# Kernel tuning notes

Hardware: AMD Instinct MI355X
Metric: run time of the kernel (lower is better)

## Reference

```python
import jax, jax.numpy as jnp
import numpy as np

IN_DIM, HID, OUT_DIM, BATCH, T = 512, 1024, 512, 4096, 32

def setup_inputs() -> dict:
    key = jax.random.key(0)
    ks = jax.random.split(key, 7)
    s_in = 1.0 / np.sqrt(IN_DIM)
    s_h = 1.0 / np.sqrt(HID)
    return {
        "x": jax.random.normal(ks[0], (IN_DIM, BATCH), dtype=jnp.float32),
        "W_in": jax.random.normal(ks[1], (HID, IN_DIM), dtype=jnp.float32) * s_in,
        "b_in": jax.random.normal(ks[2], (HID, 1), dtype=jnp.float32) * 0.01,
        "W_rec": jax.random.normal(ks[3], (HID, HID), dtype=jnp.float32) * s_h,
        "b_rec": jax.random.normal(ks[4], (HID, 1), dtype=jnp.float32) * 0.01,
        "W_out": jax.random.normal(ks[5], (OUT_DIM, HID), dtype=jnp.float32) * s_h,
        "b_out": jax.random.normal(ks[6], (OUT_DIM, 1), dtype=jnp.float32) * 0.01,
    }

def reference(x, W_in, b_in, W_rec, b_rec, W_out, b_out):
    # initial projection: [H, B]
    y0 = jax.nn.relu(W_in @ x + b_in)

    def step(h, _):
        h_next = jax.nn.relu(W_rec @ h + b_rec)
        return h_next, h_next

    h_last, hs = jax.lax.scan(step, y0, None, length=T)  # hs: [T, H, B]
    out = jax.nn.relu(W_out @ h_last + b_out)  # [O, B]
    intermediate = jnp.concatenate([y0[None], hs], axis=0)  # [T+1, H, B]
    return out, intermediate
```

## Files before the change

kernel.cpp:

```cpp
#include <hip/hip_runtime.h>
#include <hip/hip_bf16.h>

#define IN_DIM  512
#define HID     1024
#define OUT_DIM 512
#define BATCH   4096
#define T_STEPS 32

typedef __attribute__((ext_vector_type(8))) short bf16x8;
typedef __attribute__((ext_vector_type(4))) float f32x4;

__device__ inline void gload16(const void* g, void* l) {
  __builtin_amdgcn_global_load_lds(
      (const __attribute__((address_space(1))) void*)g,
      (__attribute__((address_space(3))) void*)l, 16, 0, 0);
}

__device__ inline void bload(bf16x8 &d, const __hip_bfloat16* p) {
  asm volatile("global_load_dwordx4 %0, %1, off"
               : "=&v"(d) : "v"(p) : "memory");
}

__global__ __launch_bounds__(256, 2) void gemm_bt_bias_relu(
    const __hip_bfloat16* __restrict__ A,
    const __hip_bfloat16* __restrict__ Wt,
    const float* __restrict__ bias,
    float* __restrict__ Cf,
    __hip_bfloat16* __restrict__ Cb,
    int K, int Nld, int nx)
{
  const int nwg = gridDim.x;
  const int q   = nwg >> 3;
  const int bid = blockIdx.x;
  const int swz = (bid & 7) * q + (bid >> 3);
  const int bxi = swz % nx;
  const int byi = swz / nx;
  const int brow = byi * 128;
  const int bcol = bxi * 64;

  const int tid  = threadIdx.x;
  const int lane = tid & 63;
  const int wid  = tid >> 6;
  const int wr   = wid >> 1, wc = wid & 1;
  const int l15  = lane & 15, l4 = lane >> 4;
  const int srow = lane >> 3;
  const int schunk = (lane & 7) ^ (srow & 7);

  __shared__ __hip_bfloat16 Alds[2][128 * 64];

  f32x4 acc[4][2] = {};
  const int nt = K >> 6;

  auto stageA = [&](int ti, int buf) {
    const int kt = ti << 6;
#pragma unroll
    for (int it = 0; it < 4; ++it) {
      const int rowbase = it * 32 + wid * 8;
      gload16(A + (size_t)(brow + rowbase + srow) * K + kt + schunk * 8,
              &Alds[buf][rowbase * 64]);
    }
  };

  const int Ks = K >> 5;
  const __hip_bfloat16* wt[2];
  wt[0] = Wt + (size_t)((bcol >> 4) + wc * 2 + 0) * Ks * 512 + lane * 8;
  wt[1] = Wt + (size_t)((bcol >> 4) + wc * 2 + 1) * Ks * 512 + lane * 8;

  bf16x8 bx[2][2], by[2][2];

#pragma unroll
  for (int n = 0; n < 2; ++n) {
    bload(bx[n][0], wt[n] + 0 * 512);
    bload(bx[n][1], wt[n] + 1 * 512);
  }
  __builtin_amdgcn_sched_barrier(0);
  stageA(0, 0);
  __builtin_amdgcn_sched_barrier(0);
#pragma unroll
  for (int n = 0; n < 2; ++n) {
    bload(by[n][0], wt[n] + 2 * 512);
    bload(by[n][1], wt[n] + 3 * 512);
  }
  __builtin_amdgcn_sched_barrier(0);
  stageA(1, 1);

  const int rxor = l15 & 7;

  auto iterf = [&](int ti, bf16x8 (&cb)[2][2]) {
    const int buf = ti & 1;
    if (ti < nt - 1) {
      asm volatile("s_waitcnt vmcnt(8)" ::: "memory");
    } else {
      asm volatile("s_waitcnt vmcnt(0)" ::: "memory");
    }
    __builtin_amdgcn_s_barrier();
    __builtin_amdgcn_sched_barrier(0);

    __builtin_amdgcn_s_setprio(1);
#pragma unroll
    for (int ks = 0; ks < 2; ++ks) {
      bf16x8 af[4];
      const int cp = ((ks * 4 + l4) ^ rxor) * 8;
#pragma unroll
      for (int m = 0; m < 4; ++m)
        af[m] = *(const bf16x8*)&Alds[buf][(wr * 64 + m * 16 + l15) * 64 + cp];
#pragma unroll
      for (int m = 0; m < 4; ++m)
#pragma unroll
        for (int n = 0; n < 2; ++n)
          acc[m][n] = __builtin_amdgcn_mfma_f32_16x16x32_bf16(af[m], cb[n][ks], acc[m][n], 0, 0, 0);
    }
    __builtin_amdgcn_s_setprio(0);
    __builtin_amdgcn_sched_barrier(0);

    if (ti + 2 < nt) {
      const int s0 = (ti + 2) * 2;
#pragma unroll
      for (int n = 0; n < 2; ++n) {
        bload(cb[n][0], wt[n] + (s0 + 0) * 512);
        bload(cb[n][1], wt[n] + (s0 + 1) * 512);
      }
    }

    asm volatile("s_waitcnt lgkmcnt(0)" ::: "memory");
    __builtin_amdgcn_sched_barrier(0);
    __builtin_amdgcn_s_barrier();
    __builtin_amdgcn_sched_barrier(0);
    if (ti + 2 < nt) stageA(ti + 2, buf);
  };

  for (int ti = 0; ti < nt; ti += 2) {
    iterf(ti,     bx);
    iterf(ti + 1, by);
  }

#pragma unroll
  for (int n = 0; n < 2; ++n) {
    const int i = bcol + wc * 32 + n * 16 + l15;
    const float bv = bias[i];
#pragma unroll
    for (int m = 0; m < 4; ++m) {
      const int b0 = brow + wr * 64 + m * 16 + l4 * 4;
      f32x4 v = acc[m][n];
      f32x4 o;
      o[0] = fmaxf(v[0] + bv, 0.0f);
      o[1] = fmaxf(v[1] + bv, 0.0f);
      o[2] = fmaxf(v[2] + bv, 0.0f);
      o[3] = fmaxf(v[3] + bv, 0.0f);
      __builtin_nontemporal_store(o, (f32x4*)(Cf + (size_t)i * BATCH + b0));
      if (Cb) {
        Cb[(size_t)(b0 + 0) * Nld + i] = __float2bfloat16(o[0]);
        Cb[(size_t)(b0 + 1) * Nld + i] = __float2bfloat16(o[1]);
        Cb[(size_t)(b0 + 2) * Nld + i] = __float2bfloat16(o[2]);
        Cb[(size_t)(b0 + 3) * Nld + i] = __float2bfloat16(o[3]);
      }
    }
  }
}

__global__ __launch_bounds__(256) void convert_weights_tiled(
    const float* __restrict__ w_in, const float* __restrict__ w_rec,
    const float* __restrict__ w_out,
    __hip_bfloat16* __restrict__ wi, __hip_bfloat16* __restrict__ wr,
    __hip_bfloat16* __restrict__ wo)
{
  const int c  = blockIdx.x * blockDim.x + threadIdx.x;
  const int c1 = HID * IN_DIM / 8;
  const int c2 = c1 + HID * HID / 8;
  const int c3 = c2 + OUT_DIM * HID / 8;
  const float* src; __hip_bfloat16* dst; int K, local;
  if (c < c1)      { src = w_in;  dst = wi; K = IN_DIM; local = c; }
  else if (c < c2) { src = w_rec; dst = wr; K = HID;    local = c - c1; }
  else if (c < c3) { src = w_out; dst = wo; K = HID;    local = c - c2; }
  else return;
  const int kc8 = K >> 3;
  const int i  = local / kc8;
  const int k0 = (local - i * kc8) << 3;
  const float4 a = *(const float4*)(src + (size_t)i * K + k0);
  const float4 b = *(const float4*)(src + (size_t)i * K + k0 + 4);
  union { __hip_bfloat16 h[8]; bf16x8 v; } p;
  p.h[0] = __float2bfloat16(a.x); p.h[1] = __float2bfloat16(a.y);
  p.h[2] = __float2bfloat16(a.z); p.h[3] = __float2bfloat16(a.w);
  p.h[4] = __float2bfloat16(b.x); p.h[5] = __float2bfloat16(b.y);
  p.h[6] = __float2bfloat16(b.z); p.h[7] = __float2bfloat16(b.w);
  const size_t off = ((size_t)(i >> 4) * (K >> 5) + (k0 >> 5)) * 512
                   + ((k0 >> 3) & 3) * 128 + (i & 15) * 8;
  *(bf16x8*)(dst + off) = p.v;
}

__global__ __launch_bounds__(256) void transpose_f32_bf16(
    const float* __restrict__ in, __hip_bfloat16* __restrict__ out, int R, int C)
{
  __shared__ float tile[32][33];
  const int c0 = blockIdx.x * 32, r0 = blockIdx.y * 32;
  const int tx = threadIdx.x & 31, ty = threadIdx.x >> 5;
#pragma unroll
  for (int dy = 0; dy < 32; dy += 8)
    tile[ty + dy][tx] = in[(size_t)(r0 + ty + dy) * C + c0 + tx];
  __syncthreads();
#pragma unroll
  for (int dy = 0; dy < 32; dy += 8)
    out[(size_t)(c0 + ty + dy) * R + r0 + tx] = __float2bfloat16(tile[tx][ty + dy]);
}

extern "C" void kernel_launch(void* const* d_in, const int* in_sizes, int n_in,
                              void* d_out, int out_size, void* d_ws, size_t ws_size,
                              hipStream_t stream)
{
  const float* x     = (const float*)d_in[0];
  const float* W_in  = (const float*)d_in[1];
  const float* b_in  = (const float*)d_in[2];
  const float* W_rec = (const float*)d_in[3];
  const float* b_rec = (const float*)d_in[4];
  const float* W_out = (const float*)d_in[5];
  const float* b_out = (const float*)d_in[6];

  float* out0 = (float*)d_out;
  float* itm  = out0 + (size_t)OUT_DIM * BATCH;

  __hip_bfloat16* xT = (__hip_bfloat16*)d_ws;
  __hip_bfloat16* Wi = xT + (size_t)BATCH * IN_DIM;
  __hip_bfloat16* Wr = Wi + (size_t)HID * IN_DIM;
  __hip_bfloat16* Wo = Wr + (size_t)HID * HID;
  __hip_bfloat16* h0 = Wo + (size_t)OUT_DIM * HID;
  __hip_bfloat16* h1 = h0 + (size_t)BATCH * HID;

  transpose_f32_bf16<<<dim3(BATCH / 32, IN_DIM / 32), 256, 0, stream>>>(x, xT, IN_DIM, BATCH);
  {
    const int nC = (HID * IN_DIM + HID * HID + OUT_DIM * HID) / 8;
    convert_weights_tiled<<<(nC + 255) / 256, 256, 0, stream>>>(
        W_in, W_rec, W_out, Wi, Wr, Wo);
  }

  gemm_bt_bias_relu<<<(HID / 64) * (BATCH / 128), 256, 0, stream>>>(
      xT, Wi, b_in, itm, h0, IN_DIM, HID, HID / 64);

  __hip_bfloat16* cur = h0;
  __hip_bfloat16* nxt = h1;
  for (int t = 0; t < T_STEPS; ++t) {
    float* dst = itm + (size_t)(t + 1) * HID * BATCH;
    gemm_bt_bias_relu<<<(HID / 64) * (BATCH / 128), 256, 0, stream>>>(
        cur, Wr, b_rec, dst, nxt, HID, HID, HID / 64);
    __hip_bfloat16* tmp = cur; cur = nxt; nxt = tmp;
  }

  gemm_bt_bias_relu<<<(OUT_DIM / 64) * (BATCH / 128), 256, 0, stream>>>(
      cur, Wo, b_out, out0, (__hip_bfloat16*)nullptr, HID, 0, OUT_DIM / 64);
}
```

Baseline: 503.6 us.

## Store activations in MFMA-fragment layout and load both operands directly to registers

The bf16 activation buffers (the transposed input and the hidden states) are now written in the same fragment-tiled layout already used for the weights. The GEMM can therefore load both A and B fragments straight from global memory into registers, which removes the LDS staging, the swizzle and the workgroup barriers. The warp tiling changes so that each wave owns 32 rows by 64 columns. The cost is more global loads per wave with no LDS sharing of A across waves, plus scattered 2-byte stores in the epilogue.

Measured after the change: 584.9 us. +16.2%, slower.

```diff
diff --git a/kernel.cpp b/kernel.cpp
--- a/kernel.cpp
+++ b/kernel.cpp
@@ -10,24 +10,18 @@
 typedef __attribute__((ext_vector_type(8))) short bf16x8;
 typedef __attribute__((ext_vector_type(4))) float f32x4;
 
-__device__ inline void gload16(const void* g, void* l) {
-  __builtin_amdgcn_global_load_lds(
-      (const __attribute__((address_space(1))) void*)g,
-      (__attribute__((address_space(3))) void*)l, 16, 0, 0);
-}
-
-__device__ inline void bload(bf16x8 &d, const __hip_bfloat16* p) {
+__device__ inline void fload(bf16x8 &d, const __hip_bfloat16* p) {
   asm volatile("global_load_dwordx4 %0, %1, off"
                : "=&v"(d) : "v"(p) : "memory");
 }
 
-__global__ __launch_bounds__(256, 2) void gemm_bt_bias_relu(
-    const __hip_bfloat16* __restrict__ A,
+__global__ __launch_bounds__(256, 2) void gemm_ft(
+    const __hip_bfloat16* __restrict__ At,
     const __hip_bfloat16* __restrict__ Wt,
     const float* __restrict__ bias,
     float* __restrict__ Cf,
     __hip_bfloat16* __restrict__ Cb,
-    int K, int Nld, int nx)
+    int K, int nx)
 {
   const int nwg = gridDim.x;
   const int q   = nwg >> 3;
@@ -41,106 +35,72 @@
   const int tid  = threadIdx.x;
   const int lane = tid & 63;
   const int wid  = tid >> 6;
-  const int wr   = wid >> 1, wc = wid & 1;
   const int l15  = lane & 15, l4 = lane >> 4;
-  const int srow = lane >> 3;
-  const int schunk = (lane & 7) ^ (srow & 7);
-
-  __shared__ __hip_bfloat16 Alds[2][128 * 64];
-
-  f32x4 acc[4][2] = {};
+
+  const int Ks = K >> 5;
   const int nt = K >> 6;
 
-  auto stageA = [&](int ti, int buf) {
-    const int kt = ti << 6;
-#pragma unroll
-    for (int it = 0; it < 4; ++it) {
-      const int rowbase = it * 32 + wid * 8;
-      gload16(A + (size_t)(brow + rowbase + srow) * K + kt + schunk * 8,
-              &Alds[buf][rowbase * 64]);
-    }
+  const __hip_bfloat16* wa0 = At + (size_t)((brow >> 4) + wid * 2 + 0) * Ks * 512 + lane * 8;
+  const __hip_bfloat16* wa1 = At + (size_t)((brow >> 4) + wid * 2 + 1) * Ks * 512 + lane * 8;
+  const __hip_bfloat16* wb0 = Wt + (size_t)((bcol >> 4) + 0) * Ks * 512 + lane * 8;
+  const __hip_bfloat16* wb1 = Wt + (size_t)((bcol >> 4) + 1) * Ks * 512 + lane * 8;
+  const __hip_bfloat16* wb2 = Wt + (size_t)((bcol >> 4) + 2) * Ks * 512 + lane * 8;
+  const __hip_bfloat16* wb3 = Wt + (size_t)((bcol >> 4) + 3) * Ks * 512 + lane * 8;
+
+  f32x4 acc[2][4] = {};
+
+  bf16x8 bX[4][2], aX[2][2];
+  bf16x8 bY[4][2], aY[2][2];
+
+  auto loadTile = [&](int ti, bf16x8 (&cb)[4][2], bf16x8 (&ca)[2][2]) {
+    const int s0 = ti * 2;
+    fload(cb[0][0], wb0 + (s0 + 0) * 512); fload(cb[0][1], wb0 + (s0 + 1) * 512);
+    fload(cb[1][0], wb1 + (s0 + 0) * 512); fload(cb[1][1], wb1 + (s0 + 1) * 512);
+    fload(cb[2][0], wb2 + (s0 + 0) * 512); fload(cb[2][1], wb2 + (s0 + 1) * 512);
+    fload(cb[3][0], wb3 + (s0 + 0) * 512); fload(cb[3][1], wb3 + (s0 + 1) * 512);
+    fload(ca[0][0], wa0 + (s0 + 0) * 512); fload(ca[0][1], wa0 + (s0 + 1) * 512);
+    fload(ca[1][0], wa1 + (s0 + 0) * 512); fload(ca[1][1], wa1 + (s0 + 1) * 512);
   };
 
-  const int Ks = K >> 5;
-  const __hip_bfloat16* wt[2];
-  wt[0] = Wt + (size_t)((bcol >> 4) + wc * 2 + 0) * Ks * 512 + lane * 8;
-  wt[1] = Wt + (size_t)((bcol >> 4) + wc * 2 + 1) * Ks * 512 + lane * 8;
-
-  bf16x8 bx[2][2], by[2][2];
-
-#pragma unroll
-  for (int n = 0; n < 2; ++n) {
-    bload(bx[n][0], wt[n] + 0 * 512);
-    bload(bx[n][1], wt[n] + 1 * 512);
-  }
-  __builtin_amdgcn_sched_barrier(0);
-  stageA(0, 0);
-  __builtin_amdgcn_sched_barrier(0);
-#pragma unroll
-  for (int n = 0; n < 2; ++n) {
-    bload(by[n][0], wt[n] + 2 * 512);
-    bload(by[n][1], wt[n] + 3 * 512);
-  }
-  __builtin_amdgcn_sched_barrier(0);
-  stageA(1, 1);
-
-  const int rxor = l15 & 7;
-
-  auto iterf = [&](int ti, bf16x8 (&cb)[2][2]) {
-    const int buf = ti & 1;
+  loadTile(0, bX, aX);
+  loadTile(1, bY, aY);
+
+  auto iterf = [&](int ti, bf16x8 (&cb)[4][2], bf16x8 (&ca)[2][2]) {
     if (ti < nt - 1) {
-      asm volatile("s_waitcnt vmcnt(8)" ::: "memory");
+      asm volatile("s_waitcnt vmcnt(12)" ::: "memory");
     } else {
       asm volatile("s_waitcnt vmcnt(0)" ::: "memory");
     }
-    __builtin_amdgcn_s_barrier();
     __builtin_amdgcn_sched_barrier(0);
 
     __builtin_amdgcn_s_setprio(1);
 #pragma unroll
-    for (int ks = 0; ks < 2; ++ks) {
-      bf16x8 af[4];
-      const int cp = ((ks * 4 + l4) ^ rxor) * 8;
-#pragma unroll
-      for (int m = 0; m < 4; ++m)
-        af[m] = *(const bf16x8*)&Alds[buf][(wr * 64 + m * 16 + l15) * 64 + cp];
-#pragma unroll
-      for (int m = 0; m < 4; ++m)
-#pragma unroll
-        for (int n = 0; n < 2; ++n)
-          acc[m][n] = __builtin_amdgcn_mfma_f32_16x16x32_bf16(af[m], cb[n][ks], acc[m][n], 0, 0, 0);
-    }
+    for (int ks = 0; ks < 2; ++ks)
+#pragma unroll
+      for (int m = 0; m < 2; ++m)
+#pragma unroll
+        for (int n = 0; n < 4; ++n)
+          acc[m][n] = __builtin_amdgcn_mfma_f32_16x16x32_bf16(
+              ca[m][ks], cb[n][ks], acc[m][n], 0, 0, 0);
     __builtin_amdgcn_s_setprio(0);
     __builtin_amdgcn_sched_barrier(0);
 
-    if (ti + 2 < nt) {
-      const int s0 = (ti + 2) * 2;
-#pragma unroll
-      for (int n = 0; n < 2; ++n) {
-        bload(cb[n][0], wt[n] + (s0 + 0) * 512);
-        bload(cb[n][1], wt[n] + (s0 + 1) * 512);
-      }
-    }
-
-    asm volatile("s_waitcnt lgkmcnt(0)" ::: "memory");
-    __builtin_amdgcn_sched_barrier(0);
-    __builtin_amdgcn_s_barrier();
-    __builtin_amdgcn_sched_barrier(0);
-    if (ti + 2 < nt) stageA(ti + 2, buf);
+    if (ti + 2 < nt) loadTile(ti + 2, cb, ca);
   };
 
   for (int ti = 0; ti < nt; ti += 2) {
-    iterf(ti,     bx);
-    iterf(ti + 1, by);
-  }
-
-#pragma unroll
-  for (int n = 0; n < 2; ++n) {
-    const int i = bcol + wc * 32 + n * 16 + l15;
+    iterf(ti,     bX, aX);
+    iterf(ti + 1, bY, aY);
+  }
+
+#pragma unroll
+  for (int n = 0; n < 4; ++n) {
+    const int i = bcol + n * 16 + l15;
     const float bv = bias[i];
-#pragma unroll
-    for (int m = 0; m < 4; ++m) {
-      const int b0 = brow + wr * 64 + m * 16 + l4 * 4;
+    const int ioff = (i >> 5) * 512 + ((i >> 3) & 3) * 128 + (i & 7);
+#pragma unroll
+    for (int m = 0; m < 2; ++m) {
+      const int b0 = brow + wid * 32 + m * 16 + l4 * 4;
       f32x4 v = acc[m][n];
       f32x4 o;
       o[0] = fmaxf(v[0] + bv, 0.0f);
@@ -149,10 +109,11 @@
       o[3] = fmaxf(v[3] + bv, 0.0f);
       __builtin_nontemporal_store(o, (f32x4*)(Cf + (size_t)i * BATCH + b0));
       if (Cb) {
-        Cb[(size_t)(b0 + 0) * Nld + i] = __float2bfloat16(o[0]);
-        Cb[(size_t)(b0 + 1) * Nld + i] = __float2bfloat16(o[1]);
-        Cb[(size_t)(b0 + 2) * Nld + i] = __float2bfloat16(o[2]);
-        Cb[(size_t)(b0 + 3) * Nld + i] = __float2bfloat16(o[3]);
+        const size_t cbase = (size_t)(b0 >> 4) * 16384 + ioff + l4 * 32;
+        Cb[cbase +  0] = __float2bfloat16(o[0]);
+        Cb[cbase +  8] = __float2bfloat16(o[1]);
+        Cb[cbase + 16] = __float2bfloat16(o[2]);
+        Cb[cbase + 24] = __float2bfloat16(o[3]);
       }
     }
   }
@@ -188,19 +149,27 @@
   *(bf16x8*)(dst + off) = p.v;
 }
 
-__global__ __launch_bounds__(256) void transpose_f32_bf16(
-    const float* __restrict__ in, __hip_bfloat16* __restrict__ out, int R, int C)
+__global__ __launch_bounds__(256) void transpose_x_tiled(
+    const float* __restrict__ in, __hip_bfloat16* __restrict__ out)
 {
   __shared__ float tile[32][33];
-  const int c0 = blockIdx.x * 32, r0 = blockIdx.y * 32;
+  const int c0 = blockIdx.x * 32;
+  const int r0 = blockIdx.y * 32;
   const int tx = threadIdx.x & 31, ty = threadIdx.x >> 5;
 #pragma unroll
   for (int dy = 0; dy < 32; dy += 8)
-    tile[ty + dy][tx] = in[(size_t)(r0 + ty + dy) * C + c0 + tx];
+    tile[ty + dy][tx] = in[(size_t)(r0 + ty + dy) * BATCH + c0 + tx];
   __syncthreads();
 #pragma unroll
-  for (int dy = 0; dy < 32; dy += 8)
-    out[(size_t)(c0 + ty + dy) * R + r0 + tx] = __float2bfloat16(tile[tx][ty + dy]);
+  for (int r = 0; r < 4; ++r) {
+    const int g   = r * 256 + threadIdx.x;
+    const int f   = g >> 9;
+    const int idx = g & 511;
+    const int klocal = (idx >> 7) * 8 + (idx & 7);
+    const int blocal = f * 16 + ((idx >> 3) & 15);
+    const size_t off = ((size_t)((c0 >> 4) + f) * (IN_DIM >> 5) + (r0 >> 5)) * 512 + idx;
+    out[off] = __float2bfloat16(tile[klocal][blocal]);
+  }
 }
 
 extern "C" void kernel_launch(void* const* d_in, const int* in_sizes, int n_in,
@@ -225,25 +194,25 @@
   __hip_bfloat16* h0 = Wo + (size_t)OUT_DIM * HID;
   __hip_bfloat16* h1 = h0 + (size_t)BATCH * HID;
 
-  transpose_f32_bf16<<<dim3(BATCH / 32, IN_DIM / 32), 256, 0, stream>>>(x, xT, IN_DIM, BATCH);
+  transpose_x_tiled<<<dim3(BATCH / 32, IN_DIM / 32), 256, 0, stream>>>(x, xT);
   {
     const int nC = (HID * IN_DIM + HID * HID + OUT_DIM * HID) / 8;
     convert_weights_tiled<<<(nC + 255) / 256, 256, 0, stream>>>(
         W_in, W_rec, W_out, Wi, Wr, Wo);
   }
 
-  gemm_bt_bias_relu<<<(HID / 64) * (BATCH / 128), 256, 0, stream>>>(
-      xT, Wi, b_in, itm, h0, IN_DIM, HID, HID / 64);
+  gemm_ft<<<(HID / 64) * (BATCH / 128), 256, 0, stream>>>(
+      xT, Wi, b_in, itm, h0, IN_DIM, HID / 64);
 
   __hip_bfloat16* cur = h0;
   __hip_bfloat16* nxt = h1;
   for (int t = 0; t < T_STEPS; ++t) {
     float* dst = itm + (size_t)(t + 1) * HID * BATCH;
-    gemm_bt_bias_relu<<<(HID / 64) * (BATCH / 128), 256, 0, stream>>>(
-        cur, Wr, b_rec, dst, nxt, HID, HID, HID / 64);
+    gemm_ft<<<(HID / 64) * (BATCH / 128), 256, 0, stream>>>(
+        cur, Wr, b_rec, dst, nxt, HID, HID / 64);
     __hip_bfloat16* tmp = cur; cur = nxt; nxt = tmp;
   }
 
-  gemm_bt_bias_relu<<<(OUT_DIM / 64) * (BATCH / 128), 256, 0, stream>>>(
-      cur, Wo, b_out, out0, (__hip_bfloat16*)nullptr, HID, 0, OUT_DIM / 64);
-}
+  gemm_ft<<<(OUT_DIM / 64) * (BATCH / 128), 256, 0, stream>>>(
+      cur, Wo, b_out, out0, (__hip_bfloat16*)nullptr, HID, OUT_DIM / 64);
+}
```

## Give each wave a private A tile and drop workgroup barriers

Applied to the files above, without the earlier changes.

The GEMM now runs 128 threads (2 waves) per block in place of 4. Each wave owns a 64x64 output tile and stages its own 64 rows of A into a private LDS region. Because no wave reads LDS data written by another wave, the two s_barriers per K-step are removed and each wave relies only on its own waitcnt. The trade-off is that B fragments are no longer shared across waves, so each wave loads 4 column groups of B. This doubles register accumulators and B loads per wave, and the 2-block launch bound may reduce occupancy.

Result: slower. 560.8 us (+11.4%).

```diff
diff --git a/kernel.cpp b/kernel.cpp
--- a/kernel.cpp
+++ b/kernel.cpp
@@ -21,7 +21,7 @@
                : "=&v"(d) : "v"(p) : "memory");
 }
 
-__global__ __launch_bounds__(256, 2) void gemm_bt_bias_relu(
+__global__ __launch_bounds__(128, 2) void gemm_wa(
     const __hip_bfloat16* __restrict__ A,
     const __hip_bfloat16* __restrict__ Wt,
     const float* __restrict__ bias,
@@ -41,59 +41,56 @@
   const int tid  = threadIdx.x;
   const int lane = tid & 63;
   const int wid  = tid >> 6;
-  const int wr   = wid >> 1, wc = wid & 1;
   const int l15  = lane & 15, l4 = lane >> 4;
   const int srow = lane >> 3;
   const int schunk = (lane & 7) ^ (srow & 7);
 
-  __shared__ __hip_bfloat16 Alds[2][128 * 64];
-
-  f32x4 acc[4][2] = {};
+  __shared__ __hip_bfloat16 Alds[2][2][64 * 64];
+
+  f32x4 acc[4][4] = {};
   const int nt = K >> 6;
 
+  const __hip_bfloat16* arow = A + (size_t)(brow + wid * 64 + srow) * K + schunk * 8;
   auto stageA = [&](int ti, int buf) {
     const int kt = ti << 6;
 #pragma unroll
-    for (int it = 0; it < 4; ++it) {
-      const int rowbase = it * 32 + wid * 8;
-      gload16(A + (size_t)(brow + rowbase + srow) * K + kt + schunk * 8,
-              &Alds[buf][rowbase * 64]);
-    }
+    for (int it = 0; it < 8; ++it)
+      gload16(arow + (size_t)(it * 8) * K + kt, &Alds[wid][buf][it * 8 * 64]);
   };
 
   const int Ks = K >> 5;
-  const __hip_bfloat16* wt[2];
-  wt[0] = Wt + (size_t)((bcol >> 4) + wc * 2 + 0) * Ks * 512 + lane * 8;
-  wt[1] = Wt + (size_t)((bcol >> 4) + wc * 2 + 1) * Ks * 512 + lane * 8;
-
-  bf16x8 bx[2][2], by[2][2];
-
-#pragma unroll
-  for (int n = 0; n < 2; ++n) {
-    bload(bx[n][0], wt[n] + 0 * 512);
-    bload(bx[n][1], wt[n] + 1 * 512);
-  }
+  const __hip_bfloat16* wb0 = Wt + (size_t)((bcol >> 4) + 0) * Ks * 512 + lane * 8;
+  const __hip_bfloat16* wb1 = Wt + (size_t)((bcol >> 4) + 1) * Ks * 512 + lane * 8;
+  const __hip_bfloat16* wb2 = Wt + (size_t)((bcol >> 4) + 2) * Ks * 512 + lane * 8;
+  const __hip_bfloat16* wb3 = Wt + (size_t)((bcol >> 4) + 3) * Ks * 512 + lane * 8;
+
+  bf16x8 bx[4][2], by[4][2];
+
+  auto loadB = [&](int ti, bf16x8 (&cb)[4][2]) {
+    const int s0 = ti * 2;
+    bload(cb[0][0], wb0 + (s0 + 0) * 512); bload(cb[0][1], wb0 + (s0 + 1) * 512);
+    bload(cb[1][0], wb1 + (s0 + 0) * 512); bload(cb[1][1], wb1 + (s0 + 1) * 512);
+    bload(cb[2][0], wb2 + (s0 + 0) * 512); bload(cb[2][1], wb2 + (s0 + 1) * 512);
+    bload(cb[3][0], wb3 + (s0 + 0) * 512); bload(cb[3][1], wb3 + (s0 + 1) * 512);
+  };
+
+  loadB(0, bx);
   __builtin_amdgcn_sched_barrier(0);
   stageA(0, 0);
   __builtin_amdgcn_sched_barrier(0);
-#pragma unroll
-  for (int n = 0; n < 2; ++n) {
-    bload(by[n][0], wt[n] + 2 * 512);
-    bload(by[n][1], wt[n] + 3 * 512);
-  }
+  loadB(1, by);
   __builtin_amdgcn_sched_barrier(0);
   stageA(1, 1);
 
   const int rxor = l15 & 7;
 
-  auto iterf = [&](int ti, bf16x8 (&cb)[2][2]) {
+  auto iterf = [&](int ti, bf16x8 (&cb)[4][2]) {
     const int buf = ti & 1;
     if (ti < nt - 1) {
-      asm volatile("s_waitcnt vmcnt(8)" ::: "memory");
+      asm volatile("s_waitcnt vmcnt(16)" ::: "memory");
     } else {
       asm volatile("s_waitcnt vmcnt(0)" ::: "memory");
     }
-    __builtin_amdgcn_s_barrier();
     __builtin_amdgcn_sched_barrier(0);
 
     __builtin_amdgcn_s_setprio(1);
@@ -103,30 +100,23 @@
       const int cp = ((ks * 4 + l4) ^ rxor) * 8;
 #pragma unroll
       for (int m = 0; m < 4; ++m)
-        af[m] = *(const bf16x8*)&Alds[buf][(wr * 64 + m * 16 + l15) * 64 + cp];
+        af[m] = *(const bf16x8*)&Alds[wid][buf][(m * 16 + l15) * 64 + cp];
 #pragma unroll
       for (int m = 0; m < 4; ++m)
 #pragma unroll
-        for (int n = 0; n < 2; ++n)
-          acc[m][n] = __builtin_amdgcn_mfma_f32_16x16x32_bf16(af[m], cb[n][ks], acc[m][n], 0, 0, 0);
+        for (int n = 0; n < 4; ++n)
+          acc[m][n] = __builtin_amdgcn_mfma_f32_16x16x32_bf16(
+              af[m], cb[n][ks], acc[m][n], 0, 0, 0);
     }
     __builtin_amdgcn_s_setprio(0);
     __builtin_amdgcn_sched_barrier(0);
 
     if (ti + 2 < nt) {
-      const int s0 = (ti + 2) * 2;
-#pragma unroll
-      for (int n = 0; n < 2; ++n) {
-        bload(cb[n][0], wt[n] + (s0 + 0) * 512);
-        bload(cb[n][1], wt[n] + (s0 + 1) * 512);
-      }
-    }
-
-    asm volatile("s_waitcnt lgkmcnt(0)" ::: "memory");
-    __builtin_amdgcn_sched_barrier(0);
-    __builtin_amdgcn_s_barrier();
-    __builtin_amdgcn_sched_barrier(0);
-    if (ti + 2 < nt) stageA(ti + 2, buf);
+      loadB(ti + 2, cb);
+      asm volatile("s_waitcnt lgkmcnt(0)" ::: "memory");
+      __builtin_amdgcn_sched_barrier(0);
+      stageA(ti + 2, buf);
+    }
   };
 
   for (int ti = 0; ti < nt; ti += 2) {
@@ -135,12 +125,12 @@
   }
 
 #pragma unroll
-  for (int n = 0; n < 2; ++n) {
-    const int i = bcol + wc * 32 + n * 16 + l15;
+  for (int n = 0; n < 4; ++n) {
+    const int i = bcol + n * 16 + l15;
     const float bv = bias[i];
 #pragma unroll
     for (int m = 0; m < 4; ++m) {
-      const int b0 = brow + wr * 64 + m * 16 + l4 * 4;
+      const int b0 = brow + wid * 64 + m * 16 + l4 * 4;
       f32x4 v = acc[m][n];
       f32x4 o;
       o[0] = fmaxf(v[0] + bv, 0.0f);
@@ -232,18 +222,18 @@
         W_in, W_rec, W_out, Wi, Wr, Wo);
   }
 
-  gemm_bt_bias_relu<<<(HID / 64) * (BATCH / 128), 256, 0, stream>>>(
+  gemm_wa<<<(HID / 64) * (BATCH / 128), 128, 0, stream>>>(
       xT, Wi, b_in, itm, h0, IN_DIM, HID, HID / 64);
 
   __hip_bfloat16* cur = h0;
   __hip_bfloat16* nxt = h1;
   for (int t = 0; t < T_STEPS; ++t) {
     float* dst = itm + (size_t)(t + 1) * HID * BATCH;
-    gemm_bt_bias_relu<<<(HID / 64) * (BATCH / 128), 256, 0, stream>>>(
+    gemm_wa<<<(HID / 64) * (BATCH / 128), 128, 0, stream>>>(
         cur, Wr, b_rec, dst, nxt, HID, HID, HID / 64);
     __hip_bfloat16* tmp = cur; cur = nxt; nxt = tmp;
   }
 
-  gemm_bt_bias_relu<<<(OUT_DIM / 64) * (BATCH / 128), 256, 0, stream>>>(
+  gemm_wa<<<(OUT_DIM / 64) * (BATCH / 128), 128, 0, stream>>>(
       cur, Wo, b_out, out0, (__hip_bfloat16*)nullptr, HID, 0, OUT_DIM / 64);
 }
```
